# Kernel optimization log

Measured on AMD Instinct MI355X. Metric: run time of the kernel, lower is better.

Reference implementation:

```python
import jax, jax.numpy as jnp
import numpy as np

B = 16384          # batch
D = 1024           # input_size == hidden size of each block
L = 3              # number of hidden blocks (layer_configs)
H, Q = 4, 64       # num_heads, query_size
NKV, V = 128, 256  # num_key_values, value_size  (H*V == D for residual)
OUT = 256          # out_size
EPS = 1e-5


def layernorm(x, g, b):
    m = jnp.mean(x, axis=-1, keepdims=True)
    v = jnp.mean(jnp.square(x - m), axis=-1, keepdims=True)
    return (x - m) * jax.lax.rsqrt(v + EPS) * g + b


def setup_inputs() -> dict:
    key = jax.random.key(0)
    ks = jax.random.split(key, 16)
    scale = 1e-4  # module scales Linear / out_linear weights by 0.0001 at init
    return {
        "x": jax.random.normal(ks[0], (B, D), jnp.float32),
        # per-block Linear (stacked over L identical blocks)
        "W": jax.random.normal(ks[1], (L, D, D), jnp.float32) * scale / np.sqrt(D),
        "b": jax.random.normal(ks[2], (L, D), jnp.float32) * scale,
        # MemLayer params
        "Wq": jax.random.normal(ks[3], (L, H * Q, D), jnp.float32) / np.sqrt(D),
        "keys": jax.random.normal(ks[4], (L, NKV, Q), jnp.float32),
        "values": jax.random.normal(ks[5], (L, NKV, V), jnp.float32),
        "Wout": jax.random.normal(ks[6], (L, D, H * V), jnp.float32) * scale / np.sqrt(H * V),
        # per-block LayerNorm
        "ln_g": jnp.ones((L, D), jnp.float32),
        "ln_b": jnp.zeros((L, D), jnp.float32),
        # final head: Linear(sum(layer_configs)=L*D -> OUT), LayerNorm, Sigmoid
        "Wf": jax.random.normal(ks[7], (OUT, L * D), jnp.float32) * scale / np.sqrt(L * D),
        "bf": jax.random.normal(ks[8], (OUT,), jnp.float32) * scale,
        "lnf_g": jnp.ones((OUT,), jnp.float32),
        "lnf_b": jnp.zeros((OUT,), jnp.float32),
    }


def reference(x, W, b, Wq, keys, values, Wout, ln_g, ln_b, Wf, bf, lnf_g, lnf_b):
    # Dropout layers are identity at inference.
    inv_sqrt_q = 1.0 / np.sqrt(Q).astype(np.float32)
    outs = []
    h = x
    for i in range(L):
        # Linear + ReLU
        h = jax.nn.relu(h @ W[i].T + b[i])
        # MemLayer: scores = einsum('aib,ajb->aijb').sum(-1) == q @ k^T
        q = (h @ Wq[i].T).reshape(B, H, Q)
        scores = jnp.einsum('ahq,nq->ahn', q, keys[i]) * inv_sqrt_q  # (B,H,NKV)
        attn = jax.nn.softmax(scores, axis=-1)
        # einsum('aib,ajc->aijc').mean(axis=2) == attn.sum(-1)[:,:,None] * values.mean(0)
        s = jnp.sum(attn, axis=-1)              # (B,H)
        vmean = jnp.mean(values[i], axis=0)     # (V,)
        mem = (s[:, :, None] * vmean).reshape(B, H * V)
        h = mem @ Wout[i].T + h                 # out_linear + residual
        # LayerNorm (output collected for the final concat)
        h = layernorm(h, ln_g[i], ln_b[i])
        outs.append(h)
    z = jnp.concatenate(outs, axis=-1)          # (B, L*D)
    z = z @ Wf.T + bf
    z = layernorm(z, lnf_g, lnf_b)
    return jax.nn.sigmoid(z)
```

## Files before the change

kernel.cpp:

```cpp
#include <hip/hip_runtime.h>
#include <math.h>

#define EPS 1e-5f

constexpr int Bv   = 16384;
constexpr int Dv   = 1024;
constexpr int Lv   = 3;
constexpr int NKVv = 128;
constexpr int Vv   = 256;
constexpr int OUTv = 256;
constexpr int ZLD  = Lv * Dv;

typedef short bf16x8 __attribute__((ext_vector_type(8)));
typedef float f32x4  __attribute__((ext_vector_type(4)));

using gas_t = __attribute__((address_space(1))) const void;
using las_t = __attribute__((address_space(3))) void;
#define GLD_LDS16(gp, lp) \
    __builtin_amdgcn_global_load_lds((gas_t*)(gp), (las_t*)(lp), 16, 0, 0)

static __device__ __forceinline__ ushort f2bf(float f) {
    unsigned u = __float_as_uint(f);
    u = (u + 0x7fffu + ((u >> 16) & 1u)) >> 16;
    return (ushort)u;
}
static __device__ __forceinline__ ushort f2h(float f) {
    return __builtin_bit_cast(ushort, (_Float16)f);
}
static __device__ __forceinline__ float h2f(ushort u) {
    return (float)__builtin_bit_cast(_Float16, u);
}

__global__ void vmean_kernel(const float* __restrict__ values,
                             float* __restrict__ vmean) {
    const int i = blockIdx.x, t = threadIdx.x;
    const float* vals = values + (size_t)i * NKVv * Vv;
    float s = 0.f;
    for (int n = 0; n < NKVv; ++n) s += vals[n * Vv + t];
    vmean[i * Vv + t] = s * (1.0f / NKVv);
}

__global__ void cvec_kernel(const float* __restrict__ vmean,
                            const float* __restrict__ Wout,
                            float* __restrict__ cvec) {
    const int w = threadIdx.x >> 6, lane = threadIdx.x & 63;
    const int r = blockIdx.x * 8 + w;
    const int i = r >> 10;
    const float4 mv = *(const float4*)&vmean[i * Vv + lane * 4];
    const float* row = Wout + (size_t)r * 1024;
    float acc = 0.f;
#pragma unroll
    for (int c = 0; c < 4; ++c) {
        const float4 rv = *(const float4*)&row[c * 256 + lane * 4];
        acc += mv.x * rv.x + mv.y * rv.y + mv.z * rv.z + mv.w * rv.w;
    }
#pragma unroll
    for (int o = 1; o < 64; o <<= 1) acc += __shfl_xor(acc, o, 64);
    if (lane == 0) cvec[r] = acc;
}

__global__ void wprep(const float* __restrict__ W,
                      const float* __restrict__ lng,
                      const float* __restrict__ lnb,
                      ushort* __restrict__ Wb,
                      float* __restrict__ ub, float* __restrict__ vb) {
    __shared__ float rs[8];
    const int row = blockIdx.x;
    const int i = row >> 10, n = row & 1023;
    const int t = threadIdx.x, lane = t & 63, wv = t >> 6;
    const float* Wr = W + (size_t)row * 1024;
    const float4 w4 = *(const float4*)&Wr[t * 4];
    float4 g4 = make_float4(1.f, 1.f, 1.f, 1.f);
    float4 b4 = make_float4(0.f, 0.f, 0.f, 0.f);
    if (i > 0) {
        g4 = *(const float4*)&lng[(i - 1) * 1024 + t * 4];
        b4 = *(const float4*)&lnb[(i - 1) * 1024 + t * 4];
    }
    const float s0 = w4.x * g4.x, s1 = w4.y * g4.y, s2 = w4.z * g4.z, s3 = w4.w * g4.w;
    ushort4 o = {f2bf(s0), f2bf(s1), f2bf(s2), f2bf(s3)};
    *(ushort4*)&Wb[(size_t)row * 1024 + t * 4] = o;
    float su = s0 + s1 + s2 + s3;
    float sv = w4.x * b4.x + w4.y * b4.y + w4.z * b4.z + w4.w * b4.w;
#pragma unroll
    for (int d = 1; d < 64; d <<= 1) {
        su += __shfl_xor(su, d, 64);
        sv += __shfl_xor(sv, d, 64);
    }
    if (lane == 0) { rs[wv * 2] = su; rs[wv * 2 + 1] = sv; }
    __syncthreads();
    if (t == 0 && i > 0) {
        ub[(i - 1) * 1024 + n] = rs[0] + rs[2] + rs[4] + rs[6];
        vb[(i - 1) * 1024 + n] = rs[1] + rs[3] + rs[5] + rs[7];
    }
}

__global__ void wfprep(const float* __restrict__ Wf,
                       const float* __restrict__ lng,
                       const float* __restrict__ lnb,
                       ushort* __restrict__ Wfb,
                       float* __restrict__ uf, float* __restrict__ vf) {
    __shared__ float rs[8];
    const int bid = blockIdx.x;
    const int i = bid >> 8, n = bid & 255;
    const int t = threadIdx.x, lane = t & 63, wv = t >> 6;
    const size_t base = (size_t)n * ZLD + i * 1024 + t * 4;
    const float4 w4 = *(const float4*)&Wf[base];
    const float4 g4 = *(const float4*)&lng[i * 1024 + t * 4];
    const float4 b4 = *(const float4*)&lnb[i * 1024 + t * 4];
    const float s0 = w4.x * g4.x, s1 = w4.y * g4.y, s2 = w4.z * g4.z, s3 = w4.w * g4.w;
    ushort4 o = {f2bf(s0), f2bf(s1), f2bf(s2), f2bf(s3)};
    *(ushort4*)&Wfb[base] = o;
    float su = s0 + s1 + s2 + s3;
    float sv = w4.x * b4.x + w4.y * b4.y + w4.z * b4.z + w4.w * b4.w;
#pragma unroll
    for (int d = 1; d < 64; d <<= 1) {
        su += __shfl_xor(su, d, 64);
        sv += __shfl_xor(sv, d, 64);
    }
    if (lane == 0) { rs[wv * 2] = su; rs[wv * 2 + 1] = sv; }
    __syncthreads();
    if (t == 0) {
        uf[i * 256 + n] = rs[0] + rs[2] + rs[4] + rs[6];
        vf[i * 256 + n] = rs[1] + rs[3] + rs[5] + rs[7];
    }
}

__global__ void conv_x(const float* __restrict__ x, ushort* __restrict__ z) {
    const int t = blockIdx.x * 256 + threadIdx.x;
    const int row = t >> 7, c8 = (t & 127) << 3;
    const float4 v0 = *(const float4*)&x[(size_t)row * 1024 + c8];
    const float4 v1 = *(const float4*)&x[(size_t)row * 1024 + c8 + 4];
    ushort4 o0 = {f2bf(v0.x), f2bf(v0.y), f2bf(v0.z), f2bf(v0.w)};
    ushort4 o1 = {f2bf(v1.x), f2bf(v1.y), f2bf(v1.z), f2bf(v1.w)};
    ushort* p = z + (size_t)row * ZLD + 2048 + c8;
    *(ushort4*)p       = o0;
    *(ushort4*)(p + 4) = o1;
}

#define READ_A(QR, DD)                                                        \
    do { _Pragma("unroll")                                                    \
        for (int mf = 0; mf < 4; ++mf) {                                      \
            const int _o = (DD) * 16384 + (QR) * 8192 + (arow_l + mf * 16) * 64; \
            aR[mf][0] = *(const bf16x8*)&As[_o + ck0];                        \
            aR[mf][1] = *(const bf16x8*)&As[_o + ck1];                        \
        } } while (0)

#define READ_B(QC, DD, BR)                                                    \
    do { _Pragma("unroll")                                                    \
        for (int nf = 0; nf < 2; ++nf) {                                      \
            const int _o = (DD) * 16384 + (QC) * 8192 + (brow_l + nf * 16) * 64; \
            BR[nf][0] = *(const bf16x8*)&Bs[_o + ck0];                        \
            BR[nf][1] = *(const bf16x8*)&Bs[_o + ck1];                        \
        } } while (0)

#define STAGE_A(KT, H, DD)                                                    \
    do { const ushort* _p = gAs + (size_t)((H) * 128 + w16) * lda + (KT) * 64; \
         ushort* _l = As + (DD) * 16384 + (H) * 8192 + w16 * 64;              \
         GLD_LDS16(_p, _l);                                                   \
         GLD_LDS16(_p + (size_t)8 * lda, _l + 512); } while (0)

#define STAGE_B(KT, H, DD)                                                    \
    do { const ushort* _p = gBs + (size_t)((H) * 128 + w16) * ldb + (KT) * 64; \
         ushort* _l = Bs + (DD) * 16384 + (H) * 8192 + w16 * 64;              \
         GLD_LDS16(_p, _l);                                                   \
         GLD_LDS16(_p + (size_t)8 * ldb, _l + 512); } while (0)

#define MFMA_Q(QR, QC, BR)                                                    \
    do { __builtin_amdgcn_s_setprio(1);                                       \
        _Pragma("unroll")                                                     \
        for (int mf = 0; mf < 4; ++mf) {                                      \
            _Pragma("unroll")                                                 \
            for (int nf = 0; nf < 2; ++nf) {                                  \
                acc[QR][QC][mf][nf] = __builtin_amdgcn_mfma_f32_16x16x32_bf16( \
                    aR[mf][0], BR[nf][0], acc[QR][QC][mf][nf], 0, 0, 0);      \
                acc[QR][QC][mf][nf] = __builtin_amdgcn_mfma_f32_16x16x32_bf16( \
                    aR[mf][1], BR[nf][1], acc[QR][QC][mf][nf], 0, 0, 0);      \
            }                                                                 \
        }                                                                     \
        __builtin_amdgcn_s_setprio(0); } while (0)

template<int MODE>
__global__ __launch_bounds__(512, 1)
void gemm256(const ushort* __restrict__ A, int lda,
             const ushort* __restrict__ Bw, int ldb,
             const float* __restrict__ bias,
             const float* __restrict__ cvec,
             const float* __restrict__ u_,
             const float* __restrict__ v_,
             const float2* __restrict__ pstats_in,
             float2* __restrict__ mrout,
             void* __restrict__ Cv, int ldc,
             int NT, int ksplit,
             float2* __restrict__ pstats_out) {
    __shared__ __align__(16) char smem[139264];
    ushort* As = (ushort*)smem;
    ushort* Bs = (ushort*)(smem + 65536);
    float2* mrs = (float2*)(smem + 137216);
    const int tid  = threadIdx.x;
    const int lane = tid & 63;
    const int w    = tid >> 6;
    const int wr2  = w >> 2, wc2 = w & 3;
    const int w16  = w * 16;

    const int wg  = blockIdx.x;
    int by, bx;
    if (MODE == 1) {
        const int swz = (wg & 7) * 24 + (wg >> 3);
        by = swz & 63; bx = swz >> 6;
    } else {
        const int j = wg >> 3;
        by = (wg & 7) * 8 + (j & 7);
        bx = j >> 3;
    }
    const int m0  = by * 256;
    const int n0  = (MODE == 1) ? 0 : bx * 256;
    const int koff = (MODE == 1) ? bx * ksplit : 0;

    const int swzc = ((lane & 7) ^ ((lane >> 3) & 7)) << 3;
    const ushort* gAs = A  + (size_t)(m0 + (lane >> 3)) * lda + koff + swzc;
    const ushort* gBs = Bw + (size_t)(n0 + (lane >> 3)) * ldb + koff + swzc;

    const int arow_l = wr2 * 64 + (lane & 15);
    const int brow_l = wc2 * 32 + (lane & 15);
    const int ck0 = (((lane >> 4))     ^ (lane & 7)) << 3;
    const int ck1 = ((4 + (lane >> 4)) ^ (lane & 7)) << 3;

    f32x4 acc[2][2][4][2] = {};
    bf16x8 aR[4][2], bR0[2][2], bR1[2][2];

    const bool doMR = (MODE == 2) || (MODE == 1 && bx == 2);
    float2 myMR = make_float2(0.f, 0.f);
    if (doMR && tid < 256) {
        const float4* pp = (const float4*)(pstats_in + (((size_t)(m0 + tid)) << 4));
        float sum = 0.f, sq = 0.f;
#pragma unroll
        for (int j = 0; j < 8; ++j) {
            const float4 t4 = pp[j];
            sum += t4.x + t4.z; sq += t4.y + t4.w;
        }
        const float m = sum * (1.f / Dv);
        const float var = sq * (1.f / Dv) - m * m;
        myMR = make_float2(m, rsqrtf(var + EPS));
        if (MODE == 2) mrs[tid] = myMR;
    }
    __builtin_amdgcn_sched_barrier(0);

    STAGE_A(0, 0, 0);
    STAGE_B(0, 0, 0);
    STAGE_B(0, 1, 0);
    STAGE_A(0, 1, 0);
    asm volatile("s_waitcnt vmcnt(4)" ::: "memory");
    __builtin_amdgcn_s_barrier();

    for (int t = 0; t < NT; ++t) {
        const int d  = t & 1;
        const int e2 = d ^ 1;
        const bool pf = (t + 1) < NT;
        READ_A(0, d);
        READ_B(0, d, bR0);
        if (pf) STAGE_A(t + 1, 0, e2);
        if (pf) asm volatile("s_waitcnt vmcnt(4)" ::: "memory");
        else    asm volatile("s_waitcnt vmcnt(2)" ::: "memory");
        __builtin_amdgcn_s_barrier();
        MFMA_Q(0, 0, bR0);
        READ_B(1, d, bR1);
        if (pf) STAGE_B(t + 1, 0, e2);
        if (pf) asm volatile("s_waitcnt vmcnt(4)" ::: "memory");
        else    asm volatile("s_waitcnt vmcnt(0)" ::: "memory");
        __builtin_amdgcn_s_barrier();
        MFMA_Q(0, 1, bR1);
        READ_A(1, d);
        if (pf) STAGE_B(t + 1, 1, e2);
        MFMA_Q(1, 1, bR1);
        if (pf) STAGE_A(t + 1, 1, e2);
        if (pf) asm volatile("s_waitcnt vmcnt(4)" ::: "memory");
        __builtin_amdgcn_s_barrier();
        MFMA_Q(1, 0, bR0);
    }

    if (doMR && tid < 256 && (MODE == 1 || bx == 0)) mrout[m0 + tid] = myMR;

    const int lg4 = (lane >> 4) << 2;
    ushort* tile = (ushort*)(smem + 2048);
    if (MODE != 1) {
        float bsv[2][2], csv[2][2], uu[2][2], vv[2][2];
#pragma unroll
        for (int qc = 0; qc < 2; ++qc)
#pragma unroll
            for (int nf = 0; nf < 2; ++nf) {
                const int col = n0 + qc * 128 + wc2 * 32 + nf * 16 + (lane & 15);
                bsv[qc][nf] = bias[col];
                csv[qc][nf] = cvec[col];
                if (MODE == 2) { uu[qc][nf] = u_[col]; vv[qc][nf] = v_[col]; }
            }
        __syncthreads();
#pragma unroll
        for (int qr = 0; qr < 2; ++qr)
#pragma unroll
            for (int mf = 0; mf < 4; ++mf)
#pragma unroll
                for (int r = 0; r < 4; ++r) {
                    const int rloc = qr * 128 + wr2 * 64 + mf * 16 + lg4 + r;
                    float rw = 1.f, rmw = 0.f;
                    if (MODE == 2) {
                        const float2 q = mrs[rloc];
                        rw = q.y; rmw = q.y * q.x;
                    }
                    float sum = 0.f, sq = 0.f;
#pragma unroll
                    for (int qc = 0; qc < 2; ++qc)
#pragma unroll
                        for (int nf = 0; nf < 2; ++nf) {
                            float a = acc[qr][qc][mf][nf][r];
                            float val;
                            if (MODE == 2)
                                val = fmaf(rw, a, fmaf(-rmw, uu[qc][nf],
                                          vv[qc][nf] + bsv[qc][nf]));
                            else
                                val = a + bsv[qc][nf];
                            val = fmaxf(val, 0.f) + csv[qc][nf];
                            acc[qr][qc][mf][nf][r] = val;
                            sum += val; sq += val * val;
                        }
#pragma unroll
                    for (int o = 1; o < 16; o <<= 1) {
                        sum += __shfl_xor(sum, o, 64);
                        sq  += __shfl_xor(sq,  o, 64);
                    }
                    if ((lane & 15) == 0)
                        pstats_out[(((size_t)(m0 + rloc)) << 4) + (bx << 2) + wc2] =
                            make_float2(sum, sq);
                }
#pragma unroll
        for (int qr = 0; qr < 2; ++qr)
#pragma unroll
            for (int qc = 0; qc < 2; ++qc)
#pragma unroll
                for (int mf = 0; mf < 4; ++mf)
#pragma unroll
                    for (int nf = 0; nf < 2; ++nf)
#pragma unroll
                        for (int r = 0; r < 4; ++r) {
                            const int rloc = qr * 128 + wr2 * 64 + mf * 16 + lg4 + r;
                            const int cloc = qc * 128 + wc2 * 32 + nf * 16 + (lane & 15);
                            tile[rloc * 264 + cloc] = f2bf(acc[qr][qc][mf][nf][r]);
                        }
    } else {
        __syncthreads();
#pragma unroll
        for (int qr = 0; qr < 2; ++qr)
#pragma unroll
            for (int qc = 0; qc < 2; ++qc)
#pragma unroll
                for (int mf = 0; mf < 4; ++mf)
#pragma unroll
                    for (int nf = 0; nf < 2; ++nf)
#pragma unroll
                        for (int r = 0; r < 4; ++r) {
                            const int rloc = qr * 128 + wr2 * 64 + mf * 16 + lg4 + r;
                            const int cloc = qc * 128 + wc2 * 32 + nf * 16 + (lane & 15);
                            tile[rloc * 264 + cloc] = f2h(acc[qr][qc][mf][nf][r]);
                        }
    }
    __syncthreads();
    ushort* C16 = (MODE == 1)
        ? ((ushort*)Cv + (size_t)bx * ((size_t)Bv * OUTv))
        : (ushort*)Cv;
    for (int c = tid; c < 256 * 32; c += 512) {
        const int row = c >> 5, ch = (c & 31) << 3;
        const bf16x8 v = *(const bf16x8*)&tile[row * 264 + ch];
        *(bf16x8*)&C16[(size_t)(m0 + row) * ldc + n0 + ch] = v;
    }
}

__global__ void ln_sig_reduce(const ushort* __restrict__ ps,
                              const float2* __restrict__ mr,
                              const float* __restrict__ uf,
                              const float* __restrict__ vf,
                              const float* __restrict__ bf_,
                              const float* __restrict__ g,
                              const float* __restrict__ bb,
                              float* __restrict__ y) {
    const int lane = threadIdx.x & 63;
    const int row  = blockIdx.x * 4 + (threadIdx.x >> 6);
    const size_t base = (size_t)row * OUTv + lane * 4;
    const size_t SP = (size_t)Bv * OUTv;
    const float2 q0 = mr[row];
    const float2 q1 = mr[Bv + row];
    const float2 q2 = mr[2 * Bv + row];
    const ushort4 a0 = *(const ushort4*)&ps[base];
    const ushort4 a1 = *(const ushort4*)&ps[base + SP];
    const ushort4 a2 = *(const ushort4*)&ps[base + 2 * SP];
    const float4 u0 = *(const float4*)&uf[lane * 4];
    const float4 u1 = *(const float4*)&uf[256 + lane * 4];
    const float4 u2 = *(const float4*)&uf[512 + lane * 4];
    const float4 f0 = *(const float4*)&vf[lane * 4];
    const float4 f1 = *(const float4*)&vf[256 + lane * 4];
    const float4 f2 = *(const float4*)&vf[512 + lane * 4];
    const float4 bv4 = *(const float4*)&bf_[lane * 4];
    const float cst_x = f0.x + f1.x + f2.x + bv4.x;
    const float cst_y = f0.y + f1.y + f2.y + bv4.y;
    const float cst_z = f0.z + f1.z + f2.z + bv4.z;
    const float cst_w = f0.w + f1.w + f2.w + bv4.w;
    const float v0 = q0.y * (h2f(a0.x) - q0.x * u0.x) + q1.y * (h2f(a1.x) - q1.x * u1.x)
                   + q2.y * (h2f(a2.x) - q2.x * u2.x) + cst_x;
    const float v1 = q0.y * (h2f(a0.y) - q0.x * u0.y) + q1.y * (h2f(a1.y) - q1.x * u1.y)
                   + q2.y * (h2f(a2.y) - q2.x * u2.y) + cst_y;
    const float v2 = q0.y * (h2f(a0.z) - q0.x * u0.z) + q1.y * (h2f(a1.z) - q1.x * u1.z)
                   + q2.y * (h2f(a2.z) - q2.x * u2.z) + cst_z;
    const float v3 = q0.y * (h2f(a0.w) - q0.x * u0.w) + q1.y * (h2f(a1.w) - q1.x * u1.w)
                   + q2.y * (h2f(a2.w) - q2.x * u2.w) + cst_w;
    float s = v0 + v1 + v2 + v3;
#pragma unroll
    for (int o = 1; o < 64; o <<= 1) s += __shfl_xor(s, o, 64);
    const float mean = s * (1.f / OUTv);
    const float d0 = v0 - mean, d1 = v1 - mean, d2 = v2 - mean, d3 = v3 - mean;
    float q = d0 * d0 + d1 * d1 + d2 * d2 + d3 * d3;
#pragma unroll
    for (int o = 1; o < 64; o <<= 1) q += __shfl_xor(q, o, 64);
    const float r = rsqrtf(q * (1.f / OUTv) + EPS);
    const float4 gg = *(const float4*)&g[lane * 4];
    const float4 bv = *(const float4*)&bb[lane * 4];
    float4 o;
    const float t0 = d0 * r * gg.x + bv.x;
    const float t1 = d1 * r * gg.y + bv.y;
    const float t2 = d2 * r * gg.z + bv.z;
    const float t3 = d3 * r * gg.w + bv.w;
    o.x = 1.f / (1.f + expf(-t0));
    o.y = 1.f / (1.f + expf(-t1));
    o.z = 1.f / (1.f + expf(-t2));
    o.w = 1.f / (1.f + expf(-t3));
    *(float4*)&y[base] = o;
}

extern "C" void kernel_launch(void* const* d_in, const int* in_sizes, int n_in,
                              void* d_out, int out_size, void* d_ws, size_t ws_size,
                              hipStream_t stream) {
    const float* x      = (const float*)d_in[0];
    const float* W      = (const float*)d_in[1];
    const float* b      = (const float*)d_in[2];
    const float* values = (const float*)d_in[5];
    const float* Wout   = (const float*)d_in[6];
    const float* ln_g   = (const float*)d_in[7];
    const float* ln_b   = (const float*)d_in[8];
    const float* Wf     = (const float*)d_in[9];
    const float* bf     = (const float*)d_in[10];
    const float* lnf_g  = (const float*)d_in[11];
    const float* lnf_b  = (const float*)d_in[12];
    float* out = (float*)d_out;

    char* ws = (char*)d_ws;
    ushort* zbuf = (ushort*)ws;
    ws += (size_t)Bv * ZLD * sizeof(ushort);
    ushort* psum = (ushort*)ws;
    ws += (size_t)3 * Bv * OUTv * sizeof(ushort);
    ushort* Wb = (ushort*)ws;
    ws += (size_t)Lv * Dv * Dv * sizeof(ushort);
    ushort* Wfb = (ushort*)ws;
    ws += (size_t)OUTv * ZLD * sizeof(ushort);
    float* cvec = (float*)ws;
    ws += (size_t)Lv * Dv * sizeof(float);
    float* vmean = (float*)ws;
    ws += (size_t)Lv * Vv * sizeof(float);
    float2* psA = (float2*)ws;
    ws += (size_t)Bv * 16 * sizeof(float2);
    float2* psB = (float2*)ws;
    ws += (size_t)Bv * 16 * sizeof(float2);
    float2* mr3 = (float2*)ws;
    ws += (size_t)3 * Bv * sizeof(float2);
    float* ub = (float*)ws; ws += 2 * Dv * sizeof(float);
    float* vb = (float*)ws; ws += 2 * Dv * sizeof(float);
    float* uf = (float*)ws; ws += 3 * OUTv * sizeof(float);
    float* vf = (float*)ws; ws += 3 * OUTv * sizeof(float);

    wprep<<<Lv * Dv, 256, 0, stream>>>(W, ln_g, ln_b, Wb, ub, vb);
    wfprep<<<3 * OUTv, 256, 0, stream>>>(Wf, ln_g, ln_b, Wfb, uf, vf);
    conv_x<<<Bv * 128 / 256, 256, 0, stream>>>(x, zbuf);
    vmean_kernel<<<Lv, 256, 0, stream>>>(values, vmean);
    cvec_kernel<<<Lv * Dv / 8, 512, 0, stream>>>(vmean, Wout, cvec);

    gemm256<0><<<dim3(256), 512, 0, stream>>>(
        zbuf + 2048, ZLD, Wb, Dv,
        b, cvec, nullptr, nullptr, nullptr, nullptr,
        (void*)(zbuf + 0), ZLD, 16, 0, psA);

    gemm256<2><<<dim3(256), 512, 0, stream>>>(
        zbuf, ZLD, Wb + (size_t)Dv * Dv, Dv,
        b + Dv, cvec + Dv, ub, vb, psA, mr3,
        (void*)(zbuf + Dv), ZLD, 16, 0, psB);

    gemm256<2><<<dim3(256), 512, 0, stream>>>(
        zbuf + Dv, ZLD, Wb + (size_t)2 * Dv * Dv, Dv,
        b + 2 * Dv, cvec + 2 * Dv, ub + Dv, vb + Dv, psB, mr3 + Bv,
        (void*)(zbuf + 2 * Dv), ZLD, 16, 0, psA);

    gemm256<1><<<dim3(192), 512, 0, stream>>>(
        zbuf, ZLD, Wfb, ZLD, nullptr, nullptr, nullptr, nullptr,
        psA, mr3 + 2 * Bv,
        (void*)psum, OUTv, 16, 1024, nullptr);

    ln_sig_reduce<<<Bv / 4, 256, 0, stream>>>(psum, mr3, uf, vf, bf,
                                              lnf_g, lnf_b, out);
}
```

Baseline: 195.6 us.

## Restructure GEMM to 4 waves with 128x128 warp tiles and triple-buffered K=32 stages

Rewrites the 256x256 GEMM kernel from 8 waves (64x32 warp tiles, K=64 double buffer with interleaved quarter-tile MFMA phases) to 4 waves, each computing a 128x128 sub-tile over 32-wide K slices. Staging becomes a three-deep ring with a single barrier per iteration. Per-row LayerNorm partial stats are now written per half-tile, with 8 slots per row instead of 16. The intent is more register-level reuse per LDS read and fewer barriers. In exchange it needs 256 accumulator registers per thread, risks spills or poor MFMA/load overlap, and halves the threads issuing loads.

```diff
diff --git a/kernel.cpp b/kernel.cpp
--- a/kernel.cpp
+++ b/kernel.cpp
@@ -137,50 +137,24 @@
     *(ushort4*)(p + 4) = o1;
 }
 
-#define READ_A(QR, DD)                                                        \
+#define STAGE_A(KT, BI)                                                       \
     do { _Pragma("unroll")                                                    \
-        for (int mf = 0; mf < 4; ++mf) {                                      \
-            const int _o = (DD) * 16384 + (QR) * 8192 + (arow_l + mf * 16) * 64; \
-            aR[mf][0] = *(const bf16x8*)&As[_o + ck0];                        \
-            aR[mf][1] = *(const bf16x8*)&As[_o + ck1];                        \
+        for (int j = 0; j < 4; ++j) {                                         \
+            const ushort* _p = gAs + (size_t)(w * 64 + j * 16) * lda + (KT) * 32; \
+            ushort* _l = As + (BI) * 8192 + (w * 64 + j * 16) * 32;           \
+            GLD_LDS16(_p, _l);                                                \
         } } while (0)
 
-#define READ_B(QC, DD, BR)                                                    \
+#define STAGE_B(KT, BI)                                                       \
     do { _Pragma("unroll")                                                    \
-        for (int nf = 0; nf < 2; ++nf) {                                      \
-            const int _o = (DD) * 16384 + (QC) * 8192 + (brow_l + nf * 16) * 64; \
-            BR[nf][0] = *(const bf16x8*)&Bs[_o + ck0];                        \
-            BR[nf][1] = *(const bf16x8*)&Bs[_o + ck1];                        \
+        for (int j = 0; j < 4; ++j) {                                         \
+            const ushort* _p = gBs + (size_t)(w * 64 + j * 16) * ldb + (KT) * 32; \
+            ushort* _l = Bs + (BI) * 8192 + (w * 64 + j * 16) * 32;           \
+            GLD_LDS16(_p, _l);                                                \
         } } while (0)
 
-#define STAGE_A(KT, H, DD)                                                    \
-    do { const ushort* _p = gAs + (size_t)((H) * 128 + w16) * lda + (KT) * 64; \
-         ushort* _l = As + (DD) * 16384 + (H) * 8192 + w16 * 64;              \
-         GLD_LDS16(_p, _l);                                                   \
-         GLD_LDS16(_p + (size_t)8 * lda, _l + 512); } while (0)
-
-#define STAGE_B(KT, H, DD)                                                    \
-    do { const ushort* _p = gBs + (size_t)((H) * 128 + w16) * ldb + (KT) * 64; \
-         ushort* _l = Bs + (DD) * 16384 + (H) * 8192 + w16 * 64;              \
-         GLD_LDS16(_p, _l);                                                   \
-         GLD_LDS16(_p + (size_t)8 * ldb, _l + 512); } while (0)
-
-#define MFMA_Q(QR, QC, BR)                                                    \
-    do { __builtin_amdgcn_s_setprio(1);                                       \
-        _Pragma("unroll")                                                     \
-        for (int mf = 0; mf < 4; ++mf) {                                      \
-            _Pragma("unroll")                                                 \
-            for (int nf = 0; nf < 2; ++nf) {                                  \
-                acc[QR][QC][mf][nf] = __builtin_amdgcn_mfma_f32_16x16x32_bf16( \
-                    aR[mf][0], BR[nf][0], acc[QR][QC][mf][nf], 0, 0, 0);      \
-                acc[QR][QC][mf][nf] = __builtin_amdgcn_mfma_f32_16x16x32_bf16( \
-                    aR[mf][1], BR[nf][1], acc[QR][QC][mf][nf], 0, 0, 0);      \
-            }                                                                 \
-        }                                                                     \
-        __builtin_amdgcn_s_setprio(0); } while (0)
-
 template<int MODE>
-__global__ __launch_bounds__(512, 1)
+__global__ __launch_bounds__(256, 1)
 void gemm256(const ushort* __restrict__ A, int lda,
              const ushort* __restrict__ Bw, int ldb,
              const float* __restrict__ bias,
@@ -194,13 +168,12 @@
              float2* __restrict__ pstats_out) {
     __shared__ __align__(16) char smem[139264];
     ushort* As = (ushort*)smem;
-    ushort* Bs = (ushort*)(smem + 65536);
+    ushort* Bs = (ushort*)(smem + 49152);
     float2* mrs = (float2*)(smem + 137216);
     const int tid  = threadIdx.x;
     const int lane = tid & 63;
     const int w    = tid >> 6;
-    const int wr2  = w >> 2, wc2 = w & 3;
-    const int w16  = w * 16;
+    const int wr   = w >> 1, wc = w & 1;
 
     const int wg  = blockIdx.x;
     int by, bx;
@@ -216,25 +189,24 @@
     const int n0  = (MODE == 1) ? 0 : bx * 256;
     const int koff = (MODE == 1) ? bx * ksplit : 0;
 
-    const int swzc = ((lane & 7) ^ ((lane >> 3) & 7)) << 3;
-    const ushort* gAs = A  + (size_t)(m0 + (lane >> 3)) * lda + koff + swzc;
-    const ushort* gBs = Bw + (size_t)(n0 + (lane >> 3)) * ldb + koff + swzc;
-
-    const int arow_l = wr2 * 64 + (lane & 15);
-    const int brow_l = wc2 * 32 + (lane & 15);
-    const int ck0 = (((lane >> 4))     ^ (lane & 7)) << 3;
-    const int ck1 = ((4 + (lane >> 4)) ^ (lane & 7)) << 3;
-
-    f32x4 acc[2][2][4][2] = {};
-    bf16x8 aR[4][2], bR0[2][2], bR1[2][2];
+    const int schunk = ((lane & 3) ^ ((lane >> 3) & 3)) << 3;
+    const ushort* gAs = A  + (size_t)(m0 + (lane >> 2)) * lda + koff + schunk;
+    const ushort* gBs = Bw + (size_t)(n0 + (lane >> 2)) * ldb + koff + schunk;
+
+    const int frow = lane & 15;
+    const int ck   = (((lane >> 4) ^ ((frow >> 1) & 3))) << 3;
+    const int abase = (wr * 128 + frow) * 32 + ck;
+    const int bbase = (wc * 128 + frow) * 32 + ck;
+
+    f32x4 acc[8][8] = {};
 
     const bool doMR = (MODE == 2) || (MODE == 1 && bx == 2);
     float2 myMR = make_float2(0.f, 0.f);
-    if (doMR && tid < 256) {
-        const float4* pp = (const float4*)(pstats_in + (((size_t)(m0 + tid)) << 4));
+    if (doMR) {
+        const float4* pp = (const float4*)(pstats_in + (((size_t)(m0 + tid)) << 3));
         float sum = 0.f, sq = 0.f;
 #pragma unroll
-        for (int j = 0; j < 8; ++j) {
+        for (int j = 0; j < 4; ++j) {
             const float4 t4 = pp[j];
             sum += t4.x + t4.z; sq += t4.y + t4.w;
         }
@@ -245,128 +217,105 @@
     }
     __builtin_amdgcn_sched_barrier(0);
 
-    STAGE_A(0, 0, 0);
-    STAGE_B(0, 0, 0);
-    STAGE_B(0, 1, 0);
-    STAGE_A(0, 1, 0);
-    asm volatile("s_waitcnt vmcnt(4)" ::: "memory");
-    __builtin_amdgcn_s_barrier();
+    STAGE_A(0, 0); STAGE_B(0, 0);
+    STAGE_A(1, 1); STAGE_B(1, 1);
 
     for (int t = 0; t < NT; ++t) {
-        const int d  = t & 1;
-        const int e2 = d ^ 1;
-        const bool pf = (t + 1) < NT;
-        READ_A(0, d);
-        READ_B(0, d, bR0);
-        if (pf) STAGE_A(t + 1, 0, e2);
-        if (pf) asm volatile("s_waitcnt vmcnt(4)" ::: "memory");
-        else    asm volatile("s_waitcnt vmcnt(2)" ::: "memory");
+        if (t + 1 < NT) asm volatile("s_waitcnt vmcnt(8)" ::: "memory");
+        else            asm volatile("s_waitcnt vmcnt(0)" ::: "memory");
         __builtin_amdgcn_s_barrier();
-        MFMA_Q(0, 0, bR0);
-        READ_B(1, d, bR1);
-        if (pf) STAGE_B(t + 1, 0, e2);
-        if (pf) asm volatile("s_waitcnt vmcnt(4)" ::: "memory");
-        else    asm volatile("s_waitcnt vmcnt(0)" ::: "memory");
-        __builtin_amdgcn_s_barrier();
-        MFMA_Q(0, 1, bR1);
-        READ_A(1, d);
-        if (pf) STAGE_B(t + 1, 1, e2);
-        MFMA_Q(1, 1, bR1);
-        if (pf) STAGE_A(t + 1, 1, e2);
-        if (pf) asm volatile("s_waitcnt vmcnt(4)" ::: "memory");
-        __builtin_amdgcn_s_barrier();
-        MFMA_Q(1, 0, bR0);
-    }
-
-    if (doMR && tid < 256 && (MODE == 1 || bx == 0)) mrout[m0 + tid] = myMR;
+        if (t + 2 < NT) { STAGE_A(t + 2, (t + 2) % 3); STAGE_B(t + 2, (t + 2) % 3); }
+        const ushort* Ab = As + (t % 3) * 8192;
+        const ushort* Bb = Bs + (t % 3) * 8192;
+        bf16x8 aR[8], bR[8];
+#pragma unroll
+        for (int mf = 0; mf < 8; ++mf) aR[mf] = *(const bf16x8*)&Ab[abase + mf * 512];
+#pragma unroll
+        for (int nf = 0; nf < 8; ++nf) bR[nf] = *(const bf16x8*)&Bb[bbase + nf * 512];
+        __builtin_amdgcn_s_setprio(1);
+#pragma unroll
+        for (int mf = 0; mf < 8; ++mf)
+#pragma unroll
+            for (int nf = 0; nf < 8; ++nf)
+                acc[mf][nf] = __builtin_amdgcn_mfma_f32_16x16x32_bf16(
+                    aR[mf], bR[nf], acc[mf][nf], 0, 0, 0);
+        __builtin_amdgcn_s_setprio(0);
+    }
+
+    if (doMR && (MODE == 1 || bx == 0)) mrout[m0 + tid] = myMR;
 
     const int lg4 = (lane >> 4) << 2;
     ushort* tile = (ushort*)(smem + 2048);
     if (MODE != 1) {
-        float bsv[2][2], csv[2][2], uu[2][2], vv[2][2];
-#pragma unroll
-        for (int qc = 0; qc < 2; ++qc)
-#pragma unroll
-            for (int nf = 0; nf < 2; ++nf) {
-                const int col = n0 + qc * 128 + wc2 * 32 + nf * 16 + (lane & 15);
-                bsv[qc][nf] = bias[col];
-                csv[qc][nf] = cvec[col];
-                if (MODE == 2) { uu[qc][nf] = u_[col]; vv[qc][nf] = v_[col]; }
+        float bsv[8], csv[8], uu[8], vv[8];
+#pragma unroll
+        for (int nf = 0; nf < 8; ++nf) {
+            const int col = n0 + wc * 128 + nf * 16 + (lane & 15);
+            bsv[nf] = bias[col];
+            csv[nf] = cvec[col];
+            if (MODE == 2) { uu[nf] = u_[col]; vv[nf] = v_[col]; }
+        }
+        __syncthreads();
+#pragma unroll
+        for (int mf = 0; mf < 8; ++mf)
+#pragma unroll
+            for (int r = 0; r < 4; ++r) {
+                const int rloc = wr * 128 + mf * 16 + lg4 + r;
+                float rw = 1.f, rmw = 0.f;
+                if (MODE == 2) {
+                    const float2 q = mrs[rloc];
+                    rw = q.y; rmw = q.y * q.x;
+                }
+                float sum = 0.f, sq = 0.f;
+#pragma unroll
+                for (int nf = 0; nf < 8; ++nf) {
+                    float a = acc[mf][nf][r];
+                    float val;
+                    if (MODE == 2)
+                        val = fmaf(rw, a, fmaf(-rmw, uu[nf], vv[nf] + bsv[nf]));
+                    else
+                        val = a + bsv[nf];
+                    val = fmaxf(val, 0.f) + csv[nf];
+                    acc[mf][nf][r] = val;
+                    sum += val; sq += val * val;
+                }
+#pragma unroll
+                for (int o = 1; o < 16; o <<= 1) {
+                    sum += __shfl_xor(sum, o, 64);
+                    sq  += __shfl_xor(sq,  o, 64);
+                }
+                if ((lane & 15) == 0)
+                    pstats_out[(((size_t)(m0 + rloc)) << 3) + (bx << 1) + wc] =
+                        make_float2(sum, sq);
             }
-        __syncthreads();
-#pragma unroll
-        for (int qr = 0; qr < 2; ++qr)
-#pragma unroll
-            for (int mf = 0; mf < 4; ++mf)
+#pragma unroll
+        for (int mf = 0; mf < 8; ++mf)
+#pragma unroll
+            for (int nf = 0; nf < 8; ++nf)
 #pragma unroll
                 for (int r = 0; r < 4; ++r) {
-                    const int rloc = qr * 128 + wr2 * 64 + mf * 16 + lg4 + r;
-                    float rw = 1.f, rmw = 0.f;
-                    if (MODE == 2) {
-                        const float2 q = mrs[rloc];
-                        rw = q.y; rmw = q.y * q.x;
-                    }
-                    float sum = 0.f, sq = 0.f;
-#pragma unroll
-                    for (int qc = 0; qc < 2; ++qc)
-#pragma unroll
-                        for (int nf = 0; nf < 2; ++nf) {
-                            float a = acc[qr][qc][mf][nf][r];
-                            float val;
-                            if (MODE == 2)
-                                val = fmaf(rw, a, fmaf(-rmw, uu[qc][nf],
-                                          vv[qc][nf] + bsv[qc][nf]));
-                            else
-                                val = a + bsv[qc][nf];
-                            val = fmaxf(val, 0.f) + csv[qc][nf];
-                            acc[qr][qc][mf][nf][r] = val;
-                            sum += val; sq += val * val;
-                        }
-#pragma unroll
-                    for (int o = 1; o < 16; o <<= 1) {
-                        sum += __shfl_xor(sum, o, 64);
-                        sq  += __shfl_xor(sq,  o, 64);
-                    }
-                    if ((lane & 15) == 0)
-                        pstats_out[(((size_t)(m0 + rloc)) << 4) + (bx << 2) + wc2] =
-                            make_float2(sum, sq);
+                    const int rloc = wr * 128 + mf * 16 + lg4 + r;
+                    const int cloc = wc * 128 + nf * 16 + (lane & 15);
+                    tile[rloc * 264 + cloc] = f2bf(acc[mf][nf][r]);
                 }
-#pragma unroll
-        for (int qr = 0; qr < 2; ++qr)
-#pragma unroll
-            for (int qc = 0; qc < 2; ++qc)
-#pragma unroll
-                for (int mf = 0; mf < 4; ++mf)
-#pragma unroll
-                    for (int nf = 0; nf < 2; ++nf)
-#pragma unroll
-                        for (int r = 0; r < 4; ++r) {
-                            const int rloc = qr * 128 + wr2 * 64 + mf * 16 + lg4 + r;
-                            const int cloc = qc * 128 + wc2 * 32 + nf * 16 + (lane & 15);
-                            tile[rloc * 264 + cloc] = f2bf(acc[qr][qc][mf][nf][r]);
-                        }
     } else {
         __syncthreads();
 #pragma unroll
-        for (int qr = 0; qr < 2; ++qr)
-#pragma unroll
-            for (int qc = 0; qc < 2; ++qc)
-#pragma unroll
-                for (int mf = 0; mf < 4; ++mf)
-#pragma unroll
-                    for (int nf = 0; nf < 2; ++nf)
-#pragma unroll
-                        for (int r = 0; r < 4; ++r) {
-                            const int rloc = qr * 128 + wr2 * 64 + mf * 16 + lg4 + r;
-                            const int cloc = qc * 128 + wc2 * 32 + nf * 16 + (lane & 15);
-                            tile[rloc * 264 + cloc] = f2h(acc[qr][qc][mf][nf][r]);
-                        }
+        for (int mf = 0; mf < 8; ++mf)
+#pragma unroll
+            for (int nf = 0; nf < 8; ++nf)
+#pragma unroll
+                for (int r = 0; r < 4; ++r) {
+                    const int rloc = wr * 128 + mf * 16 + lg4 + r;
+                    const int cloc = wc * 128 + nf * 16 + (lane & 15);
+                    tile[rloc * 264 + cloc] = f2h(acc[mf][nf][r]);
+                }
     }
     __syncthreads();
     ushort* C16 = (MODE == 1)
         ? ((ushort*)Cv + (size_t)bx * ((size_t)Bv * OUTv))
         : (ushort*)Cv;
-    for (int c = tid; c < 256 * 32; c += 512) {
+    for (int c = tid; c < 256 * 32; c += 256) {
         const int row = c >> 5, ch = (c & 31) << 3;
         const bf16x8 v = *(const bf16x8*)&tile[row * 264 + ch];
         *(bf16x8*)&C16[(size_t)(m0 + row) * ldc + n0 + ch] = v;
@@ -479,25 +428,25 @@
     vmean_kernel<<<Lv, 256, 0, stream>>>(values, vmean);
     cvec_kernel<<<Lv * Dv / 8, 512, 0, stream>>>(vmean, Wout, cvec);
 
-    gemm256<0><<<dim3(256), 512, 0, stream>>>(
+    gemm256<0><<<dim3(256), 256, 0, stream>>>(
         zbuf + 2048, ZLD, Wb, Dv,
         b, cvec, nullptr, nullptr, nullptr, nullptr,
-        (void*)(zbuf + 0), ZLD, 16, 0, psA);
-
-    gemm256<2><<<dim3(256), 512, 0, stream>>>(
+        (void*)(zbuf + 0), ZLD, 32, 0, psA);
+
+    gemm256<2><<<dim3(256), 256, 0, stream>>>(
         zbuf, ZLD, Wb + (size_t)Dv * Dv, Dv,
         b + Dv, cvec + Dv, ub, vb, psA, mr3,
-        (void*)(zbuf + Dv), ZLD, 16, 0, psB);
-
-    gemm256<2><<<dim3(256), 512, 0, stream>>>(
+        (void*)(zbuf + Dv), ZLD, 32, 0, psB);
+
+    gemm256<2><<<dim3(256), 256, 0, stream>>>(
         zbuf + Dv, ZLD, Wb + (size_t)2 * Dv * Dv, Dv,
         b + 2 * Dv, cvec + 2 * Dv, ub + Dv, vb + Dv, psB, mr3 + Bv,
-        (void*)(zbuf + 2 * Dv), ZLD, 16, 0, psA);
-
-    gemm256<1><<<dim3(192), 512, 0, stream>>>(
+        (void*)(zbuf + 2 * Dv), ZLD, 32, 0, psA);
+
+    gemm256<1><<<dim3(192), 256, 0, stream>>>(
         zbuf, ZLD, Wfb, ZLD, nullptr, nullptr, nullptr, nullptr,
         psA, mr3 + 2 * Bv,
-        (void*)psum, OUTv, 16, 1024, nullptr);
+        (void*)psum, OUTv, 32, 1024, nullptr);
 
     ln_sig_reduce<<<Bv / 4, 256, 0, stream>>>(psum, mr3, uf, vf, bf,
                                               lnf_g, lnf_b, out);
```

Result: slower. 233.2 us (+19.2%).
